# Kernel tuning notes

Measured on AMD Instinct MI355X. Metric: run time of the kernel, lower is better.

The kernel has to match this reference:

```python
import jax, jax.numpy as jnp
import numpy as np

N_GRAPHS = 256
RATIO = 0.5


def setup_inputs() -> dict:
    key = jax.random.key(0)
    k0, k1, k2, k3, k4 = jax.random.split(key, 5)
    N, E, D = 100000, 1600000, 64
    x = jax.random.normal(k0, (N, D), dtype=jnp.float32)
    edge_index = jax.random.randint(k1, (2, E), 0, N, dtype=jnp.int32)
    batch = jnp.sort(jax.random.randint(k2, (N,), 0, N_GRAPHS, dtype=jnp.int32))
    # GraphConv(in_channels=64, out_channels=1) parameters
    w_rel = jax.random.normal(k3, (D,), dtype=jnp.float32) * 0.1
    b_rel = jnp.zeros((), dtype=jnp.float32)
    w_root = jax.random.normal(k4, (D,), dtype=jnp.float32) * 0.1
    return {"x": x, "edge_index": edge_index, "batch": batch,
            "w_rel": w_rel, "b_rel": b_rel, "w_root": w_root}


def reference(x, edge_index, batch, w_rel, b_rel, w_root):
    N = x.shape[0]
    src, dst = edge_index[0], edge_index[1]
    # GraphConv score: lin_rel(sum_{j in N(i)} x_j) + lin_root(x_i)
    agg = jax.ops.segment_sum(x[src], dst, num_segments=N)        # [N, D]
    score = jnp.tanh(agg @ w_rel + b_rel + x @ w_root)            # [N], SAGPool tanh
    # per-graph topk: keep k_g = ceil(ratio * n_g) highest-score nodes
    sizes = jax.ops.segment_sum(jnp.ones(N, jnp.int32), batch,
                                num_segments=N_GRAPHS)            # [G]
    k = jnp.ceil(RATIO * sizes.astype(jnp.float32)).astype(jnp.int32)
    starts = jnp.concatenate([jnp.zeros(1, jnp.int32),
                              jnp.cumsum(sizes)[:-1].astype(jnp.int32)])
    order = jnp.lexsort((-score, batch))                          # graph-major, score desc
    rank = jnp.arange(N, dtype=jnp.int32) - starts[batch[order]]  # rank within graph
    keep_sorted = rank < k[batch[order]]
    keep = jnp.zeros(N, dtype=bool).at[order].set(keep_sorted)
    # kept nodes are scaled by their tanh score; dropped nodes contribute 0
    w = jnp.where(keep, score, jnp.zeros_like(score))             # [N]
    num = jax.ops.segment_sum(x * w[:, None], batch, num_segments=N_GRAPHS)
    cnt = jax.ops.segment_sum(keep.astype(x.dtype), batch, num_segments=N_GRAPHS)
    return num / jnp.maximum(cnt, 1.0)[:, None]                   # global_mean_pool
```

## Files before the change

kernel.cpp:

```cpp
#include <hip/hip_runtime.h>

#define NGRAPHS 256
#define CHUNK   2048
#define CAPG    12288
#define NMAX    2048

__global__ __launch_bounds__(512) void k1_dot(
    const float* __restrict__ x,
    const int*   __restrict__ batch,
    const float* __restrict__ w_rel,
    const float* __restrict__ w_root,
    float* __restrict__ p, float* __restrict__ r,
    int* __restrict__ starts, int* __restrict__ ends,
    int* __restrict__ cursor, int N)
{
    int tid = threadIdx.x;
    if (blockIdx.x == 0 && tid < NGRAPHS) cursor[tid] = 0;
    int row = (int)blockIdx.x * 32 + (tid >> 4);
    int fq  = tid & 15;
    if (row >= N) return;
    if (fq == 0) {
        int b = batch[row];
        if (row == 0) {
            for (int g = 0; g < b; ++g) { starts[g] = 0; ends[g] = 0; }
            starts[b] = 0;
        } else {
            int bp = batch[row - 1];
            if (bp != b) {
                ends[bp] = row;
                for (int g = bp + 1; g < b; ++g) { starts[g] = row; ends[g] = row; }
                starts[b] = row;
            }
        }
        if (row == N - 1) {
            ends[b] = N;
            for (int g = b + 1; g < NGRAPHS; ++g) { starts[g] = N; ends[g] = N; }
        }
    }
    float4 v  = *(const float4*)(x + (size_t)row * 64 + fq * 4);
    float4 wr = ((const float4*)w_rel)[fq];
    float4 wo = ((const float4*)w_root)[fq];
    float a = v.x * wr.x + v.y * wr.y + v.z * wr.z + v.w * wr.w;
    float c = v.x * wo.x + v.y * wo.y + v.z * wo.z + v.w * wo.w;
    a += __shfl_down(a, 8); c += __shfl_down(c, 8);
    a += __shfl_down(a, 4); c += __shfl_down(c, 4);
    a += __shfl_down(a, 2); c += __shfl_down(c, 2);
    a += __shfl_down(a, 1); c += __shfl_down(c, 1);
    if (fq == 0) { p[row] = a; r[row] = c; }
}

__global__ __launch_bounds__(512) void kSc_scatter(
    const int* __restrict__ ei,
    const int* __restrict__ batch,
    const int* __restrict__ starts,
    int* __restrict__ cursor,
    unsigned* __restrict__ bucket,
    int E, int vecE)
{
    __shared__ __align__(16) unsigned stage[CHUNK];
    __shared__ unsigned char sbin[CHUNK];
    __shared__ int hist[NGRAPHS];
    __shared__ int wb[NGRAPHS];
    __shared__ int sst[NGRAPHS];

    int tid = threadIdx.x;
    if (tid < NGRAPHS) { hist[tid] = 0; sst[tid] = starts[tid]; }
    __syncthreads();

    int beg = (int)blockIdx.x * CHUNK;
    int end = min(beg + CHUNK, E);
    if (vecE) {
        const int4* s4 = (const int4*)ei;
        const int4* d4 = (const int4*)(ei + E);
        for (int i = (beg >> 2) + tid; i < (end >> 2); i += 512) {
            int4 s = s4[i];
            int4 d = d4[i];
            int o = (i << 2) - beg;
            int g0 = batch[d.x], g1 = batch[d.y], g2 = batch[d.z], g3 = batch[d.w];
            int l0 = min(d.x - sst[g0], NMAX - 1);
            int l1 = min(d.y - sst[g1], NMAX - 1);
            int l2 = min(d.z - sst[g2], NMAX - 1);
            int l3 = min(d.w - sst[g3], NMAX - 1);
            uint4 st; uchar4 sb;
            st.x = ((unsigned)s.x << 11) | (unsigned)l0; sb.x = (unsigned char)g0;
            st.y = ((unsigned)s.y << 11) | (unsigned)l1; sb.y = (unsigned char)g1;
            st.z = ((unsigned)s.z << 11) | (unsigned)l2; sb.z = (unsigned char)g2;
            st.w = ((unsigned)s.w << 11) | (unsigned)l3; sb.w = (unsigned char)g3;
            *(uint4*)&stage[o] = st;
            *(uchar4*)&sbin[o] = sb;
            atomicAdd(&hist[g0], 1);
            atomicAdd(&hist[g1], 1);
            atomicAdd(&hist[g2], 1);
            atomicAdd(&hist[g3], 1);
        }
    } else {
        for (int i = beg + tid; i < end; i += 512) {
            int s = ei[i];
            int d = ei[E + i];
            int g = batch[d];
            int l = min(d - sst[g], NMAX - 1);
            int o = i - beg;
            stage[o] = ((unsigned)s << 11) | (unsigned)l;
            sbin[o]  = (unsigned char)g;
            atomicAdd(&hist[g], 1);
        }
    }
    __syncthreads();
    if (tid < NGRAPHS) {
        int h = hist[tid];
        wb[tid] = (h > 0) ? tid * CAPG + atomicAdd(&cursor[tid], h) : 0;
    }
    __syncthreads();
    int cnt = end - beg;
    for (int o = tid; o < cnt; o += 512) {
        int b = sbin[o];
        int pos = atomicAdd(&wb[b], 1);
        if (pos < (b + 1) * CAPG) bucket[pos] = stage[o];
    }
}

__global__ __launch_bounds__(256) void kZ_zero(float* __restrict__ a, int N)
{
    int i = blockIdx.x * 256 + threadIdx.x;
    if (i < N) a[i] = 0.0f;
}
__global__ __launch_bounds__(256) void k2_scatter(
    const int* __restrict__ ei, const float* __restrict__ p,
    float* aggdot, int E)
{
    int i = blockIdx.x * 256 + threadIdx.x;
    if (i < E) unsafeAtomicAdd(&aggdot[ei[E + i]], p[ei[i]]);
}
__global__ __launch_bounds__(256) void kS_score(
    const float* __restrict__ aggdot, const float* __restrict__ r,
    const float* __restrict__ brel, float* __restrict__ score, int N)
{
    int i = blockIdx.x * 256 + threadIdx.x;
    if (i < N) score[i] = tanhf(aggdot[i] + brel[0] + r[i]);
}

__global__ __launch_bounds__(512) void kPool(
    const float* __restrict__ x,
    const float* __restrict__ p,
    const float* __restrict__ r,
    const float* __restrict__ brel,
    const unsigned* __restrict__ bucket,
    const int* __restrict__ cursor,
    const int* __restrict__ starts,
    const int* __restrict__ ends,
    const float* __restrict__ score_g,
    float* __restrict__ out)
{
    __shared__ __align__(16) float sc[NMAX];
    __shared__ float acc[NMAX];
    __shared__ int   kidx[NMAX / 2 + 64];
    __shared__ float kw[NMAX / 2 + 64];
    __shared__ float accs[8][64][4];
    __shared__ int   pctr;

    int g   = blockIdx.x;
    int tid = threadIdx.x;
    int start = starts[g];
    int n     = ends[g] - start;
    if (n > NMAX) n = NMAX;
    int k = (n + 1) >> 1;
    if (tid == 0) pctr = 0;

    if (score_g) {
        for (int i = tid; i < n; i += 512) sc[i] = score_g[start + i];
    } else {
        for (int i = tid; i < n; i += 512) acc[i] = 0.0f;
        __syncthreads();
        int lo  = g * CAPG;
        int cnt = min(cursor[g], CAPG);
        const uint4* bk4 = (const uint4*)(bucket + lo);
        int quart = cnt >> 2;
        for (int e = tid; e < quart; e += 512) {
            uint4 u = bk4[e];
            float v0 = p[u.x >> 11], v1 = p[u.y >> 11];
            float v2 = p[u.z >> 11], v3 = p[u.w >> 11];
            atomicAdd(&acc[u.x & 2047u], v0);
            atomicAdd(&acc[u.y & 2047u], v1);
            atomicAdd(&acc[u.z & 2047u], v2);
            atomicAdd(&acc[u.w & 2047u], v3);
        }
        int tail = cnt & 3;
        if (tid < tail) {
            unsigned u = bucket[lo + (quart << 2) + tid];
            atomicAdd(&acc[u & 2047u], p[u >> 11]);
        }
        __syncthreads();
        float bb = brel[0];
        for (int i = tid; i < n; i += 512)
            sc[i] = tanhf(acc[i] + bb + r[start + i]);
    }
    __syncthreads();

    int n4 = n & ~3;
    for (int i = tid; i < n; i += 512) {
        float si = sc[i];
        int rank = 0;
        int j = 0;
        for (; j < n4; j += 4) {
            float4 s4 = *(const float4*)&sc[j];
            rank += (s4.x > si) || (s4.x == si && (j + 0) < i);
            rank += (s4.y > si) || (s4.y == si && (j + 1) < i);
            rank += (s4.z > si) || (s4.z == si && (j + 2) < i);
            rank += (s4.w > si) || (s4.w == si && (j + 3) < i);
        }
        for (; j < n; ++j) {
            float sj = sc[j];
            rank += (sj > si) || (sj == si && j < i);
        }
        if (rank < k) {
            int pos = atomicAdd(&pctr, 1);
            kidx[pos] = i;
            kw[pos]   = si;
        }
    }
    __syncthreads();
    int k32 = (k + 31) & ~31;
    for (int e = k + tid; e < k32; e += 512) { kidx[e] = 0; kw[e] = 0.0f; }
    __syncthreads();

    int wg   = tid >> 6;
    int lane = tid & 63;
    int rgrp = lane >> 4;
    int fq   = lane & 15;
    float a0 = 0.0f, a1 = 0.0f, a2 = 0.0f, a3 = 0.0f;
    #pragma unroll 2
    for (int e = wg * 4 + rgrp; e < k32; e += 32) {
        float wv = kw[e];
        int row  = start + kidx[e];
        const float4 v = *(const float4*)(x + (size_t)row * 64 + fq * 4);
        a0 += v.x * wv; a1 += v.y * wv; a2 += v.z * wv; a3 += v.w * wv;
    }
    accs[wg][lane][0] = a0; accs[wg][lane][1] = a1;
    accs[wg][lane][2] = a2; accs[wg][lane][3] = a3;
    __syncthreads();
    if (tid < 64) {
        float sum = 0.0f;
        #pragma unroll
        for (int gg = 0; gg < 8; ++gg)
            #pragma unroll
            for (int rg = 0; rg < 4; ++rg)
                sum += accs[gg][rg * 16 + (tid >> 2)][tid & 3];
        out[(size_t)g * 64 + tid] = sum / fmaxf((float)k, 1.0f);
    }
}

extern "C" void kernel_launch(void* const* d_in, const int* in_sizes, int n_in,
                              void* d_out, int out_size, void* d_ws, size_t ws_size,
                              hipStream_t stream) {
    const float* x      = (const float*)d_in[0];
    const int*   ei     = (const int*)  d_in[1];
    const int*   batch  = (const int*)  d_in[2];
    const float* w_rel  = (const float*)d_in[3];
    const float* b_rel  = (const float*)d_in[4];
    const float* w_root = (const float*)d_in[5];
    float* out = (float*)d_out;

    int N = in_sizes[2];
    int E = in_sizes[1] / 2;
    int NBLKE = (E + CHUNK - 1) / CHUNK;
    int vecE  = ((E & 3) == 0);
    int dotblks = (N + 31) / 32;

    float* p      = (float*)d_ws;
    float* r      = p + (size_t)N;
    int*   starts = (int*)(r + (size_t)N);
    int*   ends   = starts + NGRAPHS;
    int*   cursor = ends + NGRAPHS;
    size_t boff = (size_t)2 * N + 3 * NGRAPHS;
    boff = (boff + 3) & ~(size_t)3;
    unsigned* bucket = (unsigned*)d_ws + boff;
    size_t need = (boff + (size_t)NGRAPHS * CAPG) * 4;

    bool binned = (need <= ws_size) && (N < (1 << 17));

    k1_dot<<<dotblks, 512, 0, stream>>>(x, batch, w_rel, w_root,
                                        p, r, starts, ends, cursor, N);
    if (binned) {
        kSc_scatter<<<NBLKE, 512, 0, stream>>>(ei, batch, starts, cursor,
                                               bucket, E, vecE);
        kPool<<<NGRAPHS, 512, 0, stream>>>(x, p, r, b_rel, bucket, cursor,
                                           starts, ends, nullptr, out);
    } else {
        float* score  = (float*)(cursor + NGRAPHS);
        float* aggdot = score + (size_t)N;
        kZ_zero<<<(N + 255) / 256, 256, 0, stream>>>(aggdot, N);
        k2_scatter<<<(E + 255) / 256, 256, 0, stream>>>(ei, p, aggdot, E);
        kS_score<<<(N + 255) / 256, 256, 0, stream>>>(aggdot, r, b_rel, score, N);
        kPool<<<NGRAPHS, 512, 0, stream>>>(x, p, r, b_rel, nullptr, nullptr,
                                           starts, ends, score, out);
    }
}
```

Before: 138.7 us.

## Replace per-graph edge binning with direct global atomic scatter of projected features

Removes the two-pass bucket scheme, where edges were binned by destination graph and then accumulated in shared memory inside the pool kernel. Edges are now scattered directly with global float atomics into a per-node aggregate, using int4-vectorized edge loads. Zeroing of that aggregate is folded into the dot kernel, and the pool kernel reads it to compute scores. This cuts a large intermediate bucket write and read and the histogram work, in exchange for 1.6M contended global atomics and a different float summation order.

```diff
diff --git a/kernel.cpp b/kernel.cpp
--- a/kernel.cpp
+++ b/kernel.cpp
@@ -1,9 +1,7 @@
 #include <hip/hip_runtime.h>
 
 #define NGRAPHS 256
-#define CHUNK   2048
-#define CAPG    12288
-#define NMAX    2048
+#define NMAX 2048
 
 __global__ __launch_bounds__(512) void k1_dot(
     const float* __restrict__ x,
@@ -11,15 +9,15 @@
     const float* __restrict__ w_rel,
     const float* __restrict__ w_root,
     float* __restrict__ p, float* __restrict__ r,
-    int* __restrict__ starts, int* __restrict__ ends,
-    int* __restrict__ cursor, int N)
+    float* __restrict__ agg,
+    int* __restrict__ starts, int* __restrict__ ends, int N)
 {
     int tid = threadIdx.x;
-    if (blockIdx.x == 0 && tid < NGRAPHS) cursor[tid] = 0;
     int row = (int)blockIdx.x * 32 + (tid >> 4);
     int fq  = tid & 15;
     if (row >= N) return;
     if (fq == 0) {
+        agg[row] = 0.0f;
         int b = batch[row];
         if (row == 0) {
             for (int g = 0; g < b; ++g) { starts[g] = 0; ends[g] = 0; }
@@ -49,110 +47,44 @@
     if (fq == 0) { p[row] = a; r[row] = c; }
 }
 
-__global__ __launch_bounds__(512) void kSc_scatter(
+__global__ __launch_bounds__(256) void k2_scatter4(
     const int* __restrict__ ei,
-    const int* __restrict__ batch,
-    const int* __restrict__ starts,
-    int* __restrict__ cursor,
-    unsigned* __restrict__ bucket,
-    int E, int vecE)
+    const float* __restrict__ p,
+    float* __restrict__ agg, int E)
 {
-    __shared__ __align__(16) unsigned stage[CHUNK];
-    __shared__ unsigned char sbin[CHUNK];
-    __shared__ int hist[NGRAPHS];
-    __shared__ int wb[NGRAPHS];
-    __shared__ int sst[NGRAPHS];
-
-    int tid = threadIdx.x;
-    if (tid < NGRAPHS) { hist[tid] = 0; sst[tid] = starts[tid]; }
-    __syncthreads();
-
-    int beg = (int)blockIdx.x * CHUNK;
-    int end = min(beg + CHUNK, E);
-    if (vecE) {
-        const int4* s4 = (const int4*)ei;
-        const int4* d4 = (const int4*)(ei + E);
-        for (int i = (beg >> 2) + tid; i < (end >> 2); i += 512) {
-            int4 s = s4[i];
-            int4 d = d4[i];
-            int o = (i << 2) - beg;
-            int g0 = batch[d.x], g1 = batch[d.y], g2 = batch[d.z], g3 = batch[d.w];
-            int l0 = min(d.x - sst[g0], NMAX - 1);
-            int l1 = min(d.y - sst[g1], NMAX - 1);
-            int l2 = min(d.z - sst[g2], NMAX - 1);
-            int l3 = min(d.w - sst[g3], NMAX - 1);
-            uint4 st; uchar4 sb;
-            st.x = ((unsigned)s.x << 11) | (unsigned)l0; sb.x = (unsigned char)g0;
-            st.y = ((unsigned)s.y << 11) | (unsigned)l1; sb.y = (unsigned char)g1;
-            st.z = ((unsigned)s.z << 11) | (unsigned)l2; sb.z = (unsigned char)g2;
-            st.w = ((unsigned)s.w << 11) | (unsigned)l3; sb.w = (unsigned char)g3;
-            *(uint4*)&stage[o] = st;
-            *(uchar4*)&sbin[o] = sb;
-            atomicAdd(&hist[g0], 1);
-            atomicAdd(&hist[g1], 1);
-            atomicAdd(&hist[g2], 1);
-            atomicAdd(&hist[g3], 1);
-        }
-    } else {
-        for (int i = beg + tid; i < end; i += 512) {
-            int s = ei[i];
-            int d = ei[E + i];
-            int g = batch[d];
-            int l = min(d - sst[g], NMAX - 1);
-            int o = i - beg;
-            stage[o] = ((unsigned)s << 11) | (unsigned)l;
-            sbin[o]  = (unsigned char)g;
-            atomicAdd(&hist[g], 1);
-        }
-    }
-    __syncthreads();
-    if (tid < NGRAPHS) {
-        int h = hist[tid];
-        wb[tid] = (h > 0) ? tid * CAPG + atomicAdd(&cursor[tid], h) : 0;
-    }
-    __syncthreads();
-    int cnt = end - beg;
-    for (int o = tid; o < cnt; o += 512) {
-        int b = sbin[o];
-        int pos = atomicAdd(&wb[b], 1);
-        if (pos < (b + 1) * CAPG) bucket[pos] = stage[o];
-    }
+    int i = (int)blockIdx.x * 256 + threadIdx.x;
+    int q = E >> 2;
+    if (i >= q) return;
+    const int4* s4 = (const int4*)ei;
+    const int4* d4 = (const int4*)(ei + E);
+    int4 s = s4[i];
+    int4 d = d4[i];
+    float v0 = p[s.x], v1 = p[s.y], v2 = p[s.z], v3 = p[s.w];
+    unsafeAtomicAdd(&agg[d.x], v0);
+    unsafeAtomicAdd(&agg[d.y], v1);
+    unsafeAtomicAdd(&agg[d.z], v2);
+    unsafeAtomicAdd(&agg[d.w], v3);
 }
 
-__global__ __launch_bounds__(256) void kZ_zero(float* __restrict__ a, int N)
+__global__ __launch_bounds__(256) void k2_scatter1(
+    const int* __restrict__ ei,
+    const float* __restrict__ p,
+    float* __restrict__ agg, int E)
 {
-    int i = blockIdx.x * 256 + threadIdx.x;
-    if (i < N) a[i] = 0.0f;
-}
-__global__ __launch_bounds__(256) void k2_scatter(
-    const int* __restrict__ ei, const float* __restrict__ p,
-    float* aggdot, int E)
-{
-    int i = blockIdx.x * 256 + threadIdx.x;
-    if (i < E) unsafeAtomicAdd(&aggdot[ei[E + i]], p[ei[i]]);
-}
-__global__ __launch_bounds__(256) void kS_score(
-    const float* __restrict__ aggdot, const float* __restrict__ r,
-    const float* __restrict__ brel, float* __restrict__ score, int N)
-{
-    int i = blockIdx.x * 256 + threadIdx.x;
-    if (i < N) score[i] = tanhf(aggdot[i] + brel[0] + r[i]);
+    int i = (int)blockIdx.x * 256 + threadIdx.x;
+    if (i < E) unsafeAtomicAdd(&agg[ei[E + i]], p[ei[i]]);
 }
 
-__global__ __launch_bounds__(512) void kPool(
+__global__ __launch_bounds__(512) void k4_pool(
     const float* __restrict__ x,
-    const float* __restrict__ p,
+    const float* __restrict__ agg,
     const float* __restrict__ r,
     const float* __restrict__ brel,
-    const unsigned* __restrict__ bucket,
-    const int* __restrict__ cursor,
     const int* __restrict__ starts,
     const int* __restrict__ ends,
-    const float* __restrict__ score_g,
     float* __restrict__ out)
 {
     __shared__ __align__(16) float sc[NMAX];
-    __shared__ float acc[NMAX];
     __shared__ int   kidx[NMAX / 2 + 64];
     __shared__ float kw[NMAX / 2 + 64];
     __shared__ float accs[8][64][4];
@@ -166,34 +98,9 @@
     int k = (n + 1) >> 1;
     if (tid == 0) pctr = 0;
 
-    if (score_g) {
-        for (int i = tid; i < n; i += 512) sc[i] = score_g[start + i];
-    } else {
-        for (int i = tid; i < n; i += 512) acc[i] = 0.0f;
-        __syncthreads();
-        int lo  = g * CAPG;
-        int cnt = min(cursor[g], CAPG);
-        const uint4* bk4 = (const uint4*)(bucket + lo);
-        int quart = cnt >> 2;
-        for (int e = tid; e < quart; e += 512) {
-            uint4 u = bk4[e];
-            float v0 = p[u.x >> 11], v1 = p[u.y >> 11];
-            float v2 = p[u.z >> 11], v3 = p[u.w >> 11];
-            atomicAdd(&acc[u.x & 2047u], v0);
-            atomicAdd(&acc[u.y & 2047u], v1);
-            atomicAdd(&acc[u.z & 2047u], v2);
-            atomicAdd(&acc[u.w & 2047u], v3);
-        }
-        int tail = cnt & 3;
-        if (tid < tail) {
-            unsigned u = bucket[lo + (quart << 2) + tid];
-            atomicAdd(&acc[u & 2047u], p[u >> 11]);
-        }
-        __syncthreads();
-        float bb = brel[0];
-        for (int i = tid; i < n; i += 512)
-            sc[i] = tanhf(acc[i] + bb + r[start + i]);
-    }
+    float bb = brel[0];
+    for (int i = tid; i < n; i += 512)
+        sc[i] = tanhf(agg[start + i] + bb + r[start + i]);
     __syncthreads();
 
     int n4 = n & ~3;
@@ -262,36 +169,21 @@
 
     int N = in_sizes[2];
     int E = in_sizes[1] / 2;
-    int NBLKE = (E + CHUNK - 1) / CHUNK;
-    int vecE  = ((E & 3) == 0);
     int dotblks = (N + 31) / 32;
 
     float* p      = (float*)d_ws;
     float* r      = p + (size_t)N;
-    int*   starts = (int*)(r + (size_t)N);
+    float* agg    = r + (size_t)N;
+    int*   starts = (int*)(agg + (size_t)N);
     int*   ends   = starts + NGRAPHS;
-    int*   cursor = ends + NGRAPHS;
-    size_t boff = (size_t)2 * N + 3 * NGRAPHS;
-    boff = (boff + 3) & ~(size_t)3;
-    unsigned* bucket = (unsigned*)d_ws + boff;
-    size_t need = (boff + (size_t)NGRAPHS * CAPG) * 4;
-
-    bool binned = (need <= ws_size) && (N < (1 << 17));
 
     k1_dot<<<dotblks, 512, 0, stream>>>(x, batch, w_rel, w_root,
-                                        p, r, starts, ends, cursor, N);
-    if (binned) {
-        kSc_scatter<<<NBLKE, 512, 0, stream>>>(ei, batch, starts, cursor,
-                                               bucket, E, vecE);
-        kPool<<<NGRAPHS, 512, 0, stream>>>(x, p, r, b_rel, bucket, cursor,
-                                           starts, ends, nullptr, out);
+                                        p, r, agg, starts, ends, N);
+    if ((E & 3) == 0) {
+        int q = E >> 2;
+        k2_scatter4<<<(q + 255) / 256, 256, 0, stream>>>(ei, p, agg, E);
     } else {
-        float* score  = (float*)(cursor + NGRAPHS);
-        float* aggdot = score + (size_t)N;
-        kZ_zero<<<(N + 255) / 256, 256, 0, stream>>>(aggdot, N);
-        k2_scatter<<<(E + 255) / 256, 256, 0, stream>>>(ei, p, aggdot, E);
-        kS_score<<<(N + 255) / 256, 256, 0, stream>>>(aggdot, r, b_rel, score, N);
-        kPool<<<NGRAPHS, 512, 0, stream>>>(x, p, r, b_rel, nullptr, nullptr,
-                                           starts, ends, score, out);
+        k2_scatter1<<<(E + 255) / 256, 256, 0, stream>>>(ei, p, agg, E);
     }
+    k4_pool<<<NGRAPHS, 512, 0, stream>>>(x, agg, r, b_rel, starts, ends, out);
 }
```

Result: slower. 189.4 us (+36.5%).
